# Optimization experiments

Measured on AMD Instinct MI355X. Metric: run time of the kernel, lower is better.

The kernel has to match this reference:

```python
import jax, jax.numpy as jnp
import numpy as np

H = 256          # hidden_dim
NH = 4           # num_heads
HD = H // NH     # head_dim = 64
EPS = 1e-5


def _ln(x, g, b):
    m = jnp.mean(x, axis=-1, keepdims=True)
    v = jnp.mean(jnp.square(x - m), axis=-1, keepdims=True)
    return (x - m) * jax.lax.rsqrt(v + EPS) * g + b


def _mha1(q_in, kv_in, in_proj_w, in_proj_b, out_w, out_b):
    # Single-query / single-key multihead attention (seq_len == 1 on both sides).
    # q_in, kv_in: [B, H]
    Wq, Wk, Wv = jnp.split(in_proj_w, 3, axis=0)   # each [H, H]
    bq, bk, bv = jnp.split(in_proj_b, 3, axis=0)
    B = q_in.shape[0]
    q = (q_in @ Wq.T + bq).reshape(B, NH, HD)
    k = (kv_in @ Wk.T + bk).reshape(B, NH, HD)
    v = (kv_in @ Wv.T + bv).reshape(B, NH, HD)
    scores = jnp.sum(q * k, axis=-1, keepdims=True) / jnp.sqrt(jnp.float32(HD))  # [B,NH,1]
    w = jax.nn.softmax(scores, axis=-1)  # softmax over 1 key -> all ones
    out = (w * v).reshape(B, H)
    return out @ out_w.T + out_b


def setup_inputs() -> dict:
    key = jax.random.key(0)
    ks = jax.random.split(key, 16)
    B, BIO, TXT, NC = 65536, 32, 768, 2
    s = lambda n: 1.0 / np.sqrt(n)
    return {
        "bio": jax.random.normal(ks[0], (B, BIO), jnp.float32),
        "text": jax.random.normal(ks[1], (B, TXT), jnp.float32),
        "bio_w": jax.random.normal(ks[2], (H, BIO), jnp.float32) * s(BIO),
        "bio_b": jnp.zeros((H,), jnp.float32),
        "text_w": jax.random.normal(ks[3], (H, TXT), jnp.float32) * s(TXT),
        "text_b": jnp.zeros((H,), jnp.float32),
        "ln_bio_g": jnp.ones((H,), jnp.float32),
        "ln_bio_b": jnp.zeros((H,), jnp.float32),
        "ln_text_g": jnp.ones((H,), jnp.float32),
        "ln_text_b": jnp.zeros((H,), jnp.float32),
        "in_proj_w": jax.random.normal(ks[4], (3 * H, H), jnp.float32) * s(H),
        "in_proj_b": jnp.zeros((3 * H,), jnp.float32),
        "out_w": jax.random.normal(ks[5], (H, H), jnp.float32) * s(H),
        "out_b": jnp.zeros((H,), jnp.float32),
        "cls1_w": jax.random.normal(ks[6], (H, 2 * H), jnp.float32) * s(2 * H),
        "cls1_b": jnp.zeros((H,), jnp.float32),
        "cls_ln_g": jnp.ones((H,), jnp.float32),
        "cls_ln_b": jnp.zeros((H,), jnp.float32),
        "cls2_w": jax.random.normal(ks[7], (NC, H), jnp.float32) * s(H),
        "cls2_b": jnp.zeros((NC,), jnp.float32),
    }


def reference(bio, text, bio_w, bio_b, text_w, text_b, ln_bio_g, ln_bio_b,
              ln_text_g, ln_text_b, in_proj_w, in_proj_b, out_w, out_b,
              cls1_w, cls1_b, cls_ln_g, cls_ln_b, cls2_w, cls2_b):
    b = _ln(bio @ bio_w.T + bio_b, ln_bio_g, ln_bio_b)      # [B, H]
    t = _ln(text @ text_w.T + text_b, ln_text_g, ln_text_b)  # [B, H]
    attn_bio = _mha1(b, t, in_proj_w, in_proj_b, out_w, out_b)
    attn_text = _mha1(t, b, in_proj_w, in_proj_b, out_w, out_b)
    fused = jnp.concatenate([attn_bio, attn_text], axis=-1)  # [B, 2H]
    h = jax.nn.relu(_ln(fused @ cls1_w.T + cls1_b, cls_ln_g, cls_ln_b))
    return h @ cls2_w.T + cls2_b
```

## Files before the change

### kernel.cpp

```cpp
#include <hip/hip_runtime.h>

typedef __attribute__((ext_vector_type(4))) float f4;
typedef __attribute__((ext_vector_type(8))) short s8;

#define EPS 1e-5f

__device__ __forceinline__ unsigned short f2bf(float f) {
    union { float f; unsigned u; } v; v.f = f;
    unsigned u = v.u;
    return (unsigned short)((u + 0x7fffu + ((u >> 16) & 1u)) >> 16);
}
__device__ __forceinline__ unsigned pack2(float a, float b) {
    return (unsigned)f2bf(a) | ((unsigned)f2bf(b) << 16);
}

__global__ __launch_bounds__(256) void k_prep_fl(const float* __restrict__ text_w,
                                                 const float* __restrict__ bio_w,
                                                 unsigned short* __restrict__ twFL,
                                                 unsigned short* __restrict__ bwFL) {
    int b = blockIdx.x, t = threadIdx.x;
    if (b < 96) {
        int idx = b * 256 + t;
        int ksg = idx >> 10;
        int rem = idx & 1023;
        int ct = rem >> 6, lane = rem & 63;
        int n  = ct * 16 + (lane & 15);
        int k0 = ksg * 32 + ((lane >> 4) << 3);
        const float* src = &text_w[n * 768 + k0];
        f4 a = *(const f4*)src, c = *(const f4*)(src + 4);
        unsigned* dst = (unsigned*)&twFL[idx * 8];
        dst[0] = pack2(a[0], a[1]); dst[1] = pack2(a[2], a[3]);
        dst[2] = pack2(c[0], c[1]); dst[3] = pack2(c[2], c[3]);
    } else {
        int idx = (b - 96) * 256 + t;
        int ct = idx >> 6, lane = idx & 63;
        int n  = ct * 16 + (lane & 15);
        int k0 = (lane >> 4) << 3;
        const float* src = &bio_w[n * 32 + k0];
        f4 a = *(const f4*)src, c = *(const f4*)(src + 4);
        unsigned* dst = (unsigned*)&bwFL[idx * 8];
        dst[0] = pack2(a[0], a[1]); dst[1] = pack2(a[2], a[3]);
        dst[2] = pack2(c[0], c[1]); dst[3] = pack2(c[2], c[3]);
    }
}

__global__ __launch_bounds__(256) void k_prep_A(const float* __restrict__ out_w,
                                                const float* __restrict__ in_proj_w,
                                                const float* __restrict__ in_proj_b,
                                                const float* __restrict__ out_b,
                                                float* __restrict__ A,
                                                float* __restrict__ cvec) {
    __shared__ float srow[256];
    __shared__ float red[256];
    int i = blockIdx.x, j = threadIdx.x;
    srow[j] = out_w[i * 256 + j];
    __syncthreads();
    float acc = 0.f;
#pragma unroll 8
    for (int k = 0; k < 256; k++)
        acc = fmaf(srow[k], in_proj_w[(512 + k) * 256 + j], acc);
    A[i * 256 + j] = acc;
    red[j] = srow[j] * in_proj_b[512 + j];
    __syncthreads();
    for (int s = 128; s > 0; s >>= 1) {
        if (j < s) red[j] += red[j + s];
        __syncthreads();
    }
    if (j == 0) cvec[i] = red[0] + out_b[i];
}

__global__ __launch_bounds__(256) void k_prep_PQ(const float* __restrict__ cls1_w,
                                                 const float* __restrict__ cls1_b,
                                                 const float* __restrict__ A,
                                                 const float* __restrict__ cvec,
                                                 const float* __restrict__ ln_text_g,
                                                 const float* __restrict__ ln_text_b,
                                                 const float* __restrict__ ln_bio_g,
                                                 const float* __restrict__ ln_bio_b,
                                                 unsigned short* __restrict__ pqFL,
                                                 float* __restrict__ dvec) {
    __shared__ float w1[256], w2[256], red[256];
    int i = blockIdx.x, j = threadIdx.x;
    w1[j] = cls1_w[i * 512 + j];
    w2[j] = cls1_w[i * 512 + 256 + j];
    __syncthreads();
    float rp = 0.f, rq = 0.f;
#pragma unroll 4
    for (int k = 0; k < 256; k++) {
        float a = A[k * 256 + j];
        rp = fmaf(w1[k], a, rp);
        rq = fmaf(w2[k], a, rq);
    }
    int ct   = i >> 4;
    int lane = (i & 15) | (((j >> 3) & 3) << 4);
    int jj   = j & 7;
    int ks1  = j >> 5;
    pqFL[(((ks1     ) * 16 + ct) * 64 + lane) * 8 + jj] = f2bf(rp * ln_text_g[j]);
    pqFL[(((ks1 + 8 ) * 16 + ct) * 64 + lane) * 8 + jj] = f2bf(rq * ln_bio_g[j]);
    red[j] = rp * ln_text_b[j] + rq * ln_bio_b[j] + (w1[j] + w2[j]) * cvec[j];
    __syncthreads();
    for (int s = 128; s > 0; s >>= 1) {
        if (j < s) red[j] += red[j + s];
        __syncthreads();
    }
    if (j == 0) dvec[i] = red[0] + cls1_b[i];
}

__global__ __launch_bounds__(256, 3) void k_main(
    const float* __restrict__ bio, const float* __restrict__ text,
    const float* __restrict__ bio_b, const float* __restrict__ text_b,
    const float* __restrict__ cls_ln_g, const float* __restrict__ cls_ln_b,
    const float* __restrict__ cls2_w, const float* __restrict__ cls2_b,
    const unsigned short* __restrict__ twFL, const unsigned short* __restrict__ bwFL,
    const unsigned short* __restrict__ pqFL, const float* __restrict__ dvec,
    float* __restrict__ out)
{
    __shared__ __align__(16) unsigned short s_n[32][520];
    __shared__ __align__(16) unsigned short s_x[32][200];
    __shared__ __align__(16) unsigned short s_b[32][40];
    __shared__ float s_red[4][32][2];

    const int tid  = threadIdx.x;
    const int w    = tid >> 6;
    const int lane = tid & 63;
    const int q    = lane >> 4;
    const int lr   = lane & 15;
    const int R0   = blockIdx.x * 32;

    f4 acc[2][4];
    float s1[2][4], s2[2][4];
    float m_[2][4], iv_[2][4];

    {
        int row = tid >> 3, c4 = tid & 7;
        f4 v = *(const f4*)&bio[(size_t)(R0 + row) * 32 + c4 * 4];
        uint2 p; p.x = pack2(v[0], v[1]); p.y = pack2(v[2], v[3]);
        *(uint2*)&s_b[row][c4 * 4] = p;
    }
    __syncthreads();

#pragma unroll
    for (int rt = 0; rt < 2; rt++)
#pragma unroll
        for (int c = 0; c < 4; c++) acc[rt][c] = (f4){0.f, 0.f, 0.f, 0.f};
    {
        s8 bfr[4];
#pragma unroll
        for (int c = 0; c < 4; c++)
            bfr[c] = *(const s8*)&bwFL[((w * 4 + c) * 64 + lane) * 8];
#pragma unroll
        for (int rt = 0; rt < 2; rt++) {
            s8 afr = *(const s8*)&s_b[rt * 16 + lr][q * 8];
#pragma unroll
            for (int c = 0; c < 4; c++)
                acc[rt][c] = __builtin_amdgcn_mfma_f32_16x16x32_bf16(afr, bfr[c], acc[rt][c], 0, 0, 0);
        }
    }
#pragma unroll
    for (int rt = 0; rt < 2; rt++)
#pragma unroll
        for (int r = 0; r < 4; r++) { s1[rt][r] = 0.f; s2[rt][r] = 0.f; }
#pragma unroll
    for (int rt = 0; rt < 2; rt++)
#pragma unroll
        for (int c = 0; c < 4; c++) {
            float bb = bio_b[w * 64 + c * 16 + lr];
#pragma unroll
            for (int r = 0; r < 4; r++) {
                float x = acc[rt][c][r] + bb;
                acc[rt][c][r] = x;
                s1[rt][r] += x; s2[rt][r] += x * x;
            }
        }
#pragma unroll
    for (int off = 1; off < 16; off <<= 1)
#pragma unroll
        for (int rt = 0; rt < 2; rt++)
#pragma unroll
            for (int r = 0; r < 4; r++) {
                s1[rt][r] += __shfl_xor(s1[rt][r], off, 64);
                s2[rt][r] += __shfl_xor(s2[rt][r], off, 64);
            }
    if (lr == 0)
#pragma unroll
        for (int rt = 0; rt < 2; rt++)
#pragma unroll
            for (int r = 0; r < 4; r++) {
                int row = rt * 16 + q * 4 + r;
                s_red[w][row][0] = s1[rt][r];
                s_red[w][row][1] = s2[rt][r];
            }
    __syncthreads();
#pragma unroll
    for (int rt = 0; rt < 2; rt++)
#pragma unroll
        for (int r = 0; r < 4; r++) {
            int row = rt * 16 + q * 4 + r;
            float t1 = s_red[0][row][0] + s_red[1][row][0] + s_red[2][row][0] + s_red[3][row][0];
            float t2 = s_red[0][row][1] + s_red[1][row][1] + s_red[2][row][1] + s_red[3][row][1];
            float mm = t1 * (1.f / 256.f);
            float vv = t2 * (1.f / 256.f) - mm * mm;
            m_[rt][r]  = mm;
            iv_[rt][r] = rsqrtf(vv + EPS);
        }
#pragma unroll
    for (int rt = 0; rt < 2; rt++)
#pragma unroll
        for (int c = 0; c < 4; c++) {
            int col = w * 64 + c * 16 + lr;
#pragma unroll
            for (int r = 0; r < 4; r++)
                s_n[rt * 16 + q * 4 + r][256 + col] = f2bf((acc[rt][c][r] - m_[rt][r]) * iv_[rt][r]);
        }

#pragma unroll
    for (int rt = 0; rt < 2; rt++)
#pragma unroll
        for (int c = 0; c < 4; c++) acc[rt][c] = (f4){0.f, 0.f, 0.f, 0.f};

    for (int kc = 0; kc < 768; kc += 192) {
        __syncthreads();
#pragma unroll
        for (int i = 0; i < 6; i++) {
            int idx = tid + i * 256;
            int row = idx / 48;
            int c4  = idx % 48;
            f4 v = *(const f4*)&text[(size_t)(R0 + row) * 768 + kc + c4 * 4];
            uint2 p; p.x = pack2(v[0], v[1]); p.y = pack2(v[2], v[3]);
            *(uint2*)&s_x[row][c4 * 4] = p;
        }
        __syncthreads();
        int ksg0 = kc >> 5;
#pragma unroll
        for (int ks = 0; ks < 6; ks++) {
            s8 bfr[4];
#pragma unroll
            for (int c = 0; c < 4; c++)
                bfr[c] = *(const s8*)&twFL[(((ksg0 + ks) * 16 + w * 4 + c) * 64 + lane) * 8];
#pragma unroll
            for (int rt = 0; rt < 2; rt++) {
                s8 afr = *(const s8*)&s_x[rt * 16 + lr][ks * 32 + q * 8];
#pragma unroll
                for (int c = 0; c < 4; c++)
                    acc[rt][c] = __builtin_amdgcn_mfma_f32_16x16x32_bf16(afr, bfr[c], acc[rt][c], 0, 0, 0);
            }
        }
    }
#pragma unroll
    for (int rt = 0; rt < 2; rt++)
#pragma unroll
        for (int r = 0; r < 4; r++) { s1[rt][r] = 0.f; s2[rt][r] = 0.f; }
#pragma unroll
    for (int rt = 0; rt < 2; rt++)
#pragma unroll
        for (int c = 0; c < 4; c++) {
            float bb = text_b[w * 64 + c * 16 + lr];
#pragma unroll
            for (int r = 0; r < 4; r++) {
                float x = acc[rt][c][r] + bb;
                acc[rt][c][r] = x;
                s1[rt][r] += x; s2[rt][r] += x * x;
            }
        }
#pragma unroll
    for (int off = 1; off < 16; off <<= 1)
#pragma unroll
        for (int rt = 0; rt < 2; rt++)
#pragma unroll
            for (int r = 0; r < 4; r++) {
                s1[rt][r] += __shfl_xor(s1[rt][r], off, 64);
                s2[rt][r] += __shfl_xor(s2[rt][r], off, 64);
            }
    __syncthreads();
    if (lr == 0)
#pragma unroll
        for (int rt = 0; rt < 2; rt++)
#pragma unroll
            for (int r = 0; r < 4; r++) {
                int row = rt * 16 + q * 4 + r;
                s_red[w][row][0] = s1[rt][r];
                s_red[w][row][1] = s2[rt][r];
            }
    __syncthreads();
#pragma unroll
    for (int rt = 0; rt < 2; rt++)
#pragma unroll
        for (int r = 0; r < 4; r++) {
            int row = rt * 16 + q * 4 + r;
            float t1 = s_red[0][row][0] + s_red[1][row][0] + s_red[2][row][0] + s_red[3][row][0];
            float t2 = s_red[0][row][1] + s_red[1][row][1] + s_red[2][row][1] + s_red[3][row][1];
            float mm = t1 * (1.f / 256.f);
            float vv = t2 * (1.f / 256.f) - mm * mm;
            m_[rt][r]  = mm;
            iv_[rt][r] = rsqrtf(vv + EPS);
        }
#pragma unroll
    for (int rt = 0; rt < 2; rt++)
#pragma unroll
        for (int c = 0; c < 4; c++) {
            int col = w * 64 + c * 16 + lr;
#pragma unroll
            for (int r = 0; r < 4; r++)
                s_n[rt * 16 + q * 4 + r][col] = f2bf((acc[rt][c][r] - m_[rt][r]) * iv_[rt][r]);
        }
    __syncthreads();

#pragma unroll
    for (int rt = 0; rt < 2; rt++)
#pragma unroll
        for (int c = 0; c < 4; c++) {
            float dv = dvec[w * 64 + c * 16 + lr];
            acc[rt][c] = (f4){dv, dv, dv, dv};
        }
#pragma unroll 4
    for (int ks = 0; ks < 16; ks++) {
        s8 bfr[4];
#pragma unroll
        for (int c = 0; c < 4; c++)
            bfr[c] = *(const s8*)&pqFL[((ks * 16 + w * 4 + c) * 64 + lane) * 8];
#pragma unroll
        for (int rt = 0; rt < 2; rt++) {
            s8 afr = *(const s8*)&s_n[rt * 16 + lr][ks * 32 + q * 8];
#pragma unroll
            for (int c = 0; c < 4; c++)
                acc[rt][c] = __builtin_amdgcn_mfma_f32_16x16x32_bf16(afr, bfr[c], acc[rt][c], 0, 0, 0);
        }
    }

#pragma unroll
    for (int rt = 0; rt < 2; rt++)
#pragma unroll
        for (int r = 0; r < 4; r++) { s1[rt][r] = 0.f; s2[rt][r] = 0.f; }
#pragma unroll
    for (int rt = 0; rt < 2; rt++)
#pragma unroll
        for (int c = 0; c < 4; c++)
#pragma unroll
            for (int r = 0; r < 4; r++) {
                float x = acc[rt][c][r];
                s1[rt][r] += x; s2[rt][r] += x * x;
            }
#pragma unroll
    for (int off = 1; off < 16; off <<= 1)
#pragma unroll
        for (int rt = 0; rt < 2; rt++)
#pragma unroll
            for (int r = 0; r < 4; r++) {
                s1[rt][r] += __shfl_xor(s1[rt][r], off, 64);
                s2[rt][r] += __shfl_xor(s2[rt][r], off, 64);
            }
    if (lr == 0)
#pragma unroll
        for (int rt = 0; rt < 2; rt++)
#pragma unroll
            for (int r = 0; r < 4; r++) {
                int row = rt * 16 + q * 4 + r;
                s_red[w][row][0] = s1[rt][r];
                s_red[w][row][1] = s2[rt][r];
            }
    __syncthreads();
#pragma unroll
    for (int rt = 0; rt < 2; rt++)
#pragma unroll
        for (int r = 0; r < 4; r++) {
            int row = rt * 16 + q * 4 + r;
            float t1 = s_red[0][row][0] + s_red[1][row][0] + s_red[2][row][0] + s_red[3][row][0];
            float t2 = s_red[0][row][1] + s_red[1][row][1] + s_red[2][row][1] + s_red[3][row][1];
            float mm = t1 * (1.f / 256.f);
            float vv = t2 * (1.f / 256.f) - mm * mm;
            m_[rt][r]  = mm;
            iv_[rt][r] = rsqrtf(vv + EPS);
        }
    float po0[2][4], po1[2][4];
#pragma unroll
    for (int rt = 0; rt < 2; rt++)
#pragma unroll
        for (int r = 0; r < 4; r++) { po0[rt][r] = 0.f; po1[rt][r] = 0.f; }
#pragma unroll
    for (int rt = 0; rt < 2; rt++)
#pragma unroll
        for (int c = 0; c < 4; c++) {
            int col = w * 64 + c * 16 + lr;
            float gg = cls_ln_g[col], bb = cls_ln_b[col];
            float c0 = cls2_w[col],   c1 = cls2_w[256 + col];
#pragma unroll
            for (int r = 0; r < 4; r++) {
                float h = fmaxf((acc[rt][c][r] - m_[rt][r]) * iv_[rt][r] * gg + bb, 0.f);
                po0[rt][r] = fmaf(h, c0, po0[rt][r]);
                po1[rt][r] = fmaf(h, c1, po1[rt][r]);
            }
        }
#pragma unroll
    for (int off = 1; off < 16; off <<= 1)
#pragma unroll
        for (int rt = 0; rt < 2; rt++)
#pragma unroll
            for (int r = 0; r < 4; r++) {
                po0[rt][r] += __shfl_xor(po0[rt][r], off, 64);
                po1[rt][r] += __shfl_xor(po1[rt][r], off, 64);
            }
    __syncthreads();
    if (lr == 0)
#pragma unroll
        for (int rt = 0; rt < 2; rt++)
#pragma unroll
            for (int r = 0; r < 4; r++) {
                int row = rt * 16 + q * 4 + r;
                s_red[w][row][0] = po0[rt][r];
                s_red[w][row][1] = po1[rt][r];
            }
    __syncthreads();
    if (tid < 64) {
        int row = tid >> 1, comp = tid & 1;
        float v = s_red[0][row][comp] + s_red[1][row][comp] +
                  s_red[2][row][comp] + s_red[3][row][comp];
        out[(size_t)(R0 + row) * 2 + comp] = v + cls2_b[comp];
    }
}

extern "C" void kernel_launch(void* const* d_in, const int* in_sizes, int n_in,
                              void* d_out, int out_size, void* d_ws, size_t ws_size,
                              hipStream_t stream) {
    const float* bio       = (const float*)d_in[0];
    const float* text      = (const float*)d_in[1];
    const float* bio_w     = (const float*)d_in[2];
    const float* bio_b     = (const float*)d_in[3];
    const float* text_w    = (const float*)d_in[4];
    const float* text_b    = (const float*)d_in[5];
    const float* ln_bio_g  = (const float*)d_in[6];
    const float* ln_bio_b  = (const float*)d_in[7];
    const float* ln_text_g = (const float*)d_in[8];
    const float* ln_text_b = (const float*)d_in[9];
    const float* in_proj_w = (const float*)d_in[10];
    const float* in_proj_b = (const float*)d_in[11];
    const float* out_w     = (const float*)d_in[12];
    const float* out_b     = (const float*)d_in[13];
    const float* cls1_w    = (const float*)d_in[14];
    const float* cls1_b    = (const float*)d_in[15];
    const float* cls_ln_g  = (const float*)d_in[16];
    const float* cls_ln_b  = (const float*)d_in[17];
    const float* cls2_w    = (const float*)d_in[18];
    const float* cls2_b    = (const float*)d_in[19];
    float* out = (float*)d_out;

    float* ws   = (float*)d_ws;
    float* A    = ws;
    float* cvec = ws + 65536;
    float* dvec = ws + 65792;
    unsigned short* us   = (unsigned short*)(ws + 66048);
    unsigned short* twFL = us;
    unsigned short* bwFL = us + 196608;
    unsigned short* pqFL = us + 204800;

    k_prep_fl<<<100, 256, 0, stream>>>(text_w, bio_w, twFL, bwFL);
    k_prep_A <<<256, 256, 0, stream>>>(out_w, in_proj_w, in_proj_b, out_b, A, cvec);
    k_prep_PQ<<<256, 256, 0, stream>>>(cls1_w, cls1_b, A, cvec,
                                       ln_text_g, ln_text_b, ln_bio_g, ln_bio_b,
                                       pqFL, dvec);

    int nrows = in_sizes[0] / 32;
    k_main<<<nrows / 32, 256, 0, stream>>>(bio, text, bio_b, text_b,
                                           cls_ln_g, cls_ln_b, cls2_w, cls2_b,
                                           twFL, bwFL, pqFL, dvec, out);
}
```

Before: 407.3 us.

## Double rows per block, prefetch text chunks into registers, merge prep kernels

The main kernel now handles 64 rows per 512-thread block, with two row-halves of four column-slice waves each. The next 192-column text chunk is prefetched into registers while the current chunk is multiplied, and text staging reuses the s_n buffer, dropping the separate s_x and s_b buffers. Bio inputs are loaded straight into MFMA fragments instead of going through LDS. The first two prep kernels are merged into one launch and some unroll factors are raised. The aim is to hide global load latency and cut launch overhead, at the cost of higher register pressure and a larger LDS footprint per block.

Measured after the change: 397.3 us. 2.5% less time.

```diff
diff --git a/kernel.cpp b/kernel.cpp
--- a/kernel.cpp
+++ b/kernel.cpp
@@ -13,11 +13,23 @@
 __device__ __forceinline__ unsigned pack2(float a, float b) {
     return (unsigned)f2bf(a) | ((unsigned)f2bf(b) << 16);
 }
-
-__global__ __launch_bounds__(256) void k_prep_fl(const float* __restrict__ text_w,
-                                                 const float* __restrict__ bio_w,
-                                                 unsigned short* __restrict__ twFL,
-                                                 unsigned short* __restrict__ bwFL) {
+__device__ __forceinline__ s8 pack8(f4 a, f4 b) {
+    union { s8 v; unsigned u[4]; } r;
+    r.u[0] = pack2(a[0], a[1]); r.u[1] = pack2(a[2], a[3]);
+    r.u[2] = pack2(b[0], b[1]); r.u[3] = pack2(b[2], b[3]);
+    return r.v;
+}
+
+__global__ __launch_bounds__(256) void k_prep1(const float* __restrict__ text_w,
+                                               const float* __restrict__ bio_w,
+                                               const float* __restrict__ out_w,
+                                               const float* __restrict__ in_proj_w,
+                                               const float* __restrict__ in_proj_b,
+                                               const float* __restrict__ out_b,
+                                               unsigned short* __restrict__ twFL,
+                                               unsigned short* __restrict__ bwFL,
+                                               float* __restrict__ A,
+                                               float* __restrict__ cvec) {
     int b = blockIdx.x, t = threadIdx.x;
     if (b < 96) {
         int idx = b * 256 + t;
@@ -31,7 +43,7 @@
         unsigned* dst = (unsigned*)&twFL[idx * 8];
         dst[0] = pack2(a[0], a[1]); dst[1] = pack2(a[2], a[3]);
         dst[2] = pack2(c[0], c[1]); dst[3] = pack2(c[2], c[3]);
-    } else {
+    } else if (b < 100) {
         int idx = (b - 96) * 256 + t;
         int ct = idx >> 6, lane = idx & 63;
         int n  = ct * 16 + (lane & 15);
@@ -41,32 +53,25 @@
         unsigned* dst = (unsigned*)&bwFL[idx * 8];
         dst[0] = pack2(a[0], a[1]); dst[1] = pack2(a[2], a[3]);
         dst[2] = pack2(c[0], c[1]); dst[3] = pack2(c[2], c[3]);
-    }
-}
-
-__global__ __launch_bounds__(256) void k_prep_A(const float* __restrict__ out_w,
-                                                const float* __restrict__ in_proj_w,
-                                                const float* __restrict__ in_proj_b,
-                                                const float* __restrict__ out_b,
-                                                float* __restrict__ A,
-                                                float* __restrict__ cvec) {
-    __shared__ float srow[256];
-    __shared__ float red[256];
-    int i = blockIdx.x, j = threadIdx.x;
-    srow[j] = out_w[i * 256 + j];
-    __syncthreads();
-    float acc = 0.f;
-#pragma unroll 8
-    for (int k = 0; k < 256; k++)
-        acc = fmaf(srow[k], in_proj_w[(512 + k) * 256 + j], acc);
-    A[i * 256 + j] = acc;
-    red[j] = srow[j] * in_proj_b[512 + j];
-    __syncthreads();
-    for (int s = 128; s > 0; s >>= 1) {
-        if (j < s) red[j] += red[j + s];
+    } else {
+        __shared__ float srow[256];
+        __shared__ float red[256];
+        int i = b - 100, j = t;
+        srow[j] = out_w[i * 256 + j];
         __syncthreads();
-    }
-    if (j == 0) cvec[i] = red[0] + out_b[i];
+        float acc = 0.f;
+#pragma unroll 16
+        for (int k = 0; k < 256; k++)
+            acc = fmaf(srow[k], in_proj_w[(512 + k) * 256 + j], acc);
+        A[i * 256 + j] = acc;
+        red[j] = srow[j] * in_proj_b[512 + j];
+        __syncthreads();
+        for (int s = 128; s > 0; s >>= 1) {
+            if (j < s) red[j] += red[j + s];
+            __syncthreads();
+        }
+        if (j == 0) cvec[i] = red[0] + out_b[i];
+    }
 }
 
 __global__ __launch_bounds__(256) void k_prep_PQ(const float* __restrict__ cls1_w,
@@ -85,7 +90,7 @@
     w2[j] = cls1_w[i * 512 + 256 + j];
     __syncthreads();
     float rp = 0.f, rq = 0.f;
-#pragma unroll 4
+#pragma unroll 8
     for (int k = 0; k < 256; k++) {
         float a = A[k * 256 + j];
         rp = fmaf(w1[k], a, rp);
@@ -106,7 +111,7 @@
     if (j == 0) dvec[i] = red[0] + cls1_b[i];
 }
 
-__global__ __launch_bounds__(256, 3) void k_main(
+__global__ __launch_bounds__(512, 4) void k_main(
     const float* __restrict__ bio, const float* __restrict__ text,
     const float* __restrict__ bio_b, const float* __restrict__ text_b,
     const float* __restrict__ cls_ln_g, const float* __restrict__ cls_ln_b,
@@ -115,46 +120,55 @@
     const unsigned short* __restrict__ pqFL, const float* __restrict__ dvec,
     float* __restrict__ out)
 {
-    __shared__ __align__(16) unsigned short s_n[32][520];
-    __shared__ __align__(16) unsigned short s_x[32][200];
-    __shared__ __align__(16) unsigned short s_b[32][40];
-    __shared__ float s_red[4][32][2];
+    __shared__ __align__(16) unsigned short s_n[64][520];
+    __shared__ float s_red[4][64][2];
 
     const int tid  = threadIdx.x;
-    const int w    = tid >> 6;
+    const int wv   = tid >> 6;
+    const int cs   = wv & 3;
+    const int rh   = wv >> 2;
     const int lane = tid & 63;
     const int q    = lane >> 4;
     const int lr   = lane & 15;
-    const int R0   = blockIdx.x * 32;
+    const int R0   = blockIdx.x * 64;
 
     f4 acc[2][4];
-    float s1[2][4], s2[2][4];
-    float m_[2][4], iv_[2][4];
-
-    {
-        int row = tid >> 3, c4 = tid & 7;
-        f4 v = *(const f4*)&bio[(size_t)(R0 + row) * 32 + c4 * 4];
-        uint2 p; p.x = pack2(v[0], v[1]); p.y = pack2(v[2], v[3]);
-        *(uint2*)&s_b[row][c4 * 4] = p;
-    }
-    __syncthreads();
+    float s1[2][4], s2[2][4], m_[2][4], iv_[2][4];
+
+    f4 bioA[2], bioB[2];
+#pragma unroll
+    for (int rt = 0; rt < 2; rt++) {
+        const float* p = &bio[(size_t)(R0 + rh * 32 + rt * 16 + lr) * 32 + q * 8];
+        bioA[rt] = *(const f4*)p;
+        bioB[rt] = *(const f4*)(p + 4);
+    }
+    s8 bfrb[4];
+#pragma unroll
+    for (int c = 0; c < 4; c++)
+        bfrb[c] = *(const s8*)&bwFL[((cs * 4 + c) * 64 + lane) * 8];
+
+    int toff[6], soff[6];
+    f4 tpre[6];
+#pragma unroll
+    for (int i = 0; i < 6; i++) {
+        int idx = tid + i * 512;
+        int row = idx / 48;
+        int c4  = idx - row * 48;
+        toff[i] = (R0 + row) * 768 + c4 * 4;
+        soff[i] = row * 520 + c4 * 4;
+        tpre[i] = *(const f4*)&text[(size_t)toff[i]];
+    }
 
 #pragma unroll
     for (int rt = 0; rt < 2; rt++)
 #pragma unroll
         for (int c = 0; c < 4; c++) acc[rt][c] = (f4){0.f, 0.f, 0.f, 0.f};
-    {
-        s8 bfr[4];
+#pragma unroll
+    for (int rt = 0; rt < 2; rt++) {
+        s8 af = pack8(bioA[rt], bioB[rt]);
 #pragma unroll
         for (int c = 0; c < 4; c++)
-            bfr[c] = *(const s8*)&bwFL[((w * 4 + c) * 64 + lane) * 8];
-#pragma unroll
-        for (int rt = 0; rt < 2; rt++) {
-            s8 afr = *(const s8*)&s_b[rt * 16 + lr][q * 8];
-#pragma unroll
-            for (int c = 0; c < 4; c++)
-                acc[rt][c] = __builtin_amdgcn_mfma_f32_16x16x32_bf16(afr, bfr[c], acc[rt][c], 0, 0, 0);
-        }
+            acc[rt][c] = __builtin_amdgcn_mfma_f32_16x16x32_bf16(af, bfrb[c], acc[rt][c], 0, 0, 0);
     }
 #pragma unroll
     for (int rt = 0; rt < 2; rt++)
@@ -164,7 +178,7 @@
     for (int rt = 0; rt < 2; rt++)
 #pragma unroll
         for (int c = 0; c < 4; c++) {
-            float bb = bio_b[w * 64 + c * 16 + lr];
+            float bb = bio_b[cs * 64 + c * 16 + lr];
 #pragma unroll
             for (int r = 0; r < 4; r++) {
                 float x = acc[rt][c][r] + bb;
@@ -186,16 +200,16 @@
         for (int rt = 0; rt < 2; rt++)
 #pragma unroll
             for (int r = 0; r < 4; r++) {
-                int row = rt * 16 + q * 4 + r;
-                s_red[w][row][0] = s1[rt][r];
-                s_red[w][row][1] = s2[rt][r];
+                int row = rh * 32 + rt * 16 + q * 4 + r;
+                s_red[cs][row][0] = s1[rt][r];
+                s_red[cs][row][1] = s2[rt][r];
             }
     __syncthreads();
 #pragma unroll
     for (int rt = 0; rt < 2; rt++)
 #pragma unroll
         for (int r = 0; r < 4; r++) {
-            int row = rt * 16 + q * 4 + r;
+            int row = rh * 32 + rt * 16 + q * 4 + r;
             float t1 = s_red[0][row][0] + s_red[1][row][0] + s_red[2][row][0] + s_red[3][row][0];
             float t2 = s_red[0][row][1] + s_red[1][row][1] + s_red[2][row][1] + s_red[3][row][1];
             float mm = t1 * (1.f / 256.f);
@@ -207,10 +221,11 @@
     for (int rt = 0; rt < 2; rt++)
 #pragma unroll
         for (int c = 0; c < 4; c++) {
-            int col = w * 64 + c * 16 + lr;
+            int col = cs * 64 + c * 16 + lr;
 #pragma unroll
             for (int r = 0; r < 4; r++)
-                s_n[rt * 16 + q * 4 + r][256 + col] = f2bf((acc[rt][c][r] - m_[rt][r]) * iv_[rt][r]);
+                s_n[rh * 32 + rt * 16 + q * 4 + r][256 + col] =
+                    f2bf((acc[rt][c][r] - m_[rt][r]) * iv_[rt][r]);
         }
 
 #pragma unroll
@@ -218,31 +233,31 @@
 #pragma unroll
         for (int c = 0; c < 4; c++) acc[rt][c] = (f4){0.f, 0.f, 0.f, 0.f};
 
-    for (int kc = 0; kc < 768; kc += 192) {
+    for (int ch = 0; ch < 4; ch++) {
+        if (ch) __syncthreads();
+#pragma unroll
+        for (int i = 0; i < 6; i++) {
+            uint2 p; p.x = pack2(tpre[i][0], tpre[i][1]); p.y = pack2(tpre[i][2], tpre[i][3]);
+            *(uint2*)&((unsigned short*)s_n)[soff[i]] = p;
+        }
+        if (ch < 3)
+#pragma unroll
+            for (int i = 0; i < 6; i++)
+                tpre[i] = *(const f4*)&text[(size_t)(toff[i] + (ch + 1) * 192)];
         __syncthreads();
-#pragma unroll
-        for (int i = 0; i < 6; i++) {
-            int idx = tid + i * 256;
-            int row = idx / 48;
-            int c4  = idx % 48;
-            f4 v = *(const f4*)&text[(size_t)(R0 + row) * 768 + kc + c4 * 4];
-            uint2 p; p.x = pack2(v[0], v[1]); p.y = pack2(v[2], v[3]);
-            *(uint2*)&s_x[row][c4 * 4] = p;
-        }
-        __syncthreads();
-        int ksg0 = kc >> 5;
+        int ksg0 = ch * 6;
 #pragma unroll
         for (int ks = 0; ks < 6; ks++) {
             s8 bfr[4];
 #pragma unroll
             for (int c = 0; c < 4; c++)
-                bfr[c] = *(const s8*)&twFL[(((ksg0 + ks) * 16 + w * 4 + c) * 64 + lane) * 8];
+                bfr[c] = *(const s8*)&twFL[(((ksg0 + ks) * 16 + cs * 4 + c) * 64 + lane) * 8];
 #pragma unroll
             for (int rt = 0; rt < 2; rt++) {
-                s8 afr = *(const s8*)&s_x[rt * 16 + lr][ks * 32 + q * 8];
+                s8 af = *(const s8*)&s_n[rh * 32 + rt * 16 + lr][ks * 32 + q * 8];
 #pragma unroll
                 for (int c = 0; c < 4; c++)
-                    acc[rt][c] = __builtin_amdgcn_mfma_f32_16x16x32_bf16(afr, bfr[c], acc[rt][c], 0, 0, 0);
+                    acc[rt][c] = __builtin_amdgcn_mfma_f32_16x16x32_bf16(af, bfr[c], acc[rt][c], 0, 0, 0);
             }
         }
     }
@@ -254,7 +269,7 @@
     for (int rt = 0; rt < 2; rt++)
 #pragma unroll
         for (int c = 0; c < 4; c++) {
-            float bb = text_b[w * 64 + c * 16 + lr];
+            float bb = text_b[cs * 64 + c * 16 + lr];
 #pragma unroll
             for (int r = 0; r < 4; r++) {
                 float x = acc[rt][c][r] + bb;
@@ -277,16 +292,16 @@
         for (int rt = 0; rt < 2; rt++)
 #pragma unroll
             for (int r = 0; r < 4; r++) {
-                int row = rt * 16 + q * 4 + r;
-                s_red[w][row][0] = s1[rt][r];
-                s_red[w][row][1] = s2[rt][r];
+                int row = rh * 32 + rt * 16 + q * 4 + r;
+                s_red[cs][row][0] = s1[rt][r];
+                s_red[cs][row][1] = s2[rt][r];
             }
     __syncthreads();
 #pragma unroll
     for (int rt = 0; rt < 2; rt++)
 #pragma unroll
         for (int r = 0; r < 4; r++) {
-            int row = rt * 16 + q * 4 + r;
+            int row = rh * 32 + rt * 16 + q * 4 + r;
             float t1 = s_red[0][row][0] + s_red[1][row][0] + s_red[2][row][0] + s_red[3][row][0];
             float t2 = s_red[0][row][1] + s_red[1][row][1] + s_red[2][row][1] + s_red[3][row][1];
             float mm = t1 * (1.f / 256.f);
@@ -298,18 +313,19 @@
     for (int rt = 0; rt < 2; rt++)
 #pragma unroll
         for (int c = 0; c < 4; c++) {
-            int col = w * 64 + c * 16 + lr;
+            int col = cs * 64 + c * 16 + lr;
 #pragma unroll
             for (int r = 0; r < 4; r++)
-                s_n[rt * 16 + q * 4 + r][col] = f2bf((acc[rt][c][r] - m_[rt][r]) * iv_[rt][r]);
-        }
-    __syncthreads();
-
-#pragma unroll
-    for (int rt = 0; rt < 2; rt++)
-#pragma unroll
-        for (int c = 0; c < 4; c++) {
-            float dv = dvec[w * 64 + c * 16 + lr];
+                s_n[rh * 32 + rt * 16 + q * 4 + r][col] =
+                    f2bf((acc[rt][c][r] - m_[rt][r]) * iv_[rt][r]);
+        }
+    __syncthreads();
+
+#pragma unroll
+    for (int rt = 0; rt < 2; rt++)
+#pragma unroll
+        for (int c = 0; c < 4; c++) {
+            float dv = dvec[cs * 64 + c * 16 + lr];
             acc[rt][c] = (f4){dv, dv, dv, dv};
         }
 #pragma unroll 4
@@ -317,13 +333,13 @@
         s8 bfr[4];
 #pragma unroll
         for (int c = 0; c < 4; c++)
-            bfr[c] = *(const s8*)&pqFL[((ks * 16 + w * 4 + c) * 64 + lane) * 8];
+            bfr[c] = *(const s8*)&pqFL[((ks * 16 + cs * 4 + c) * 64 + lane) * 8];
 #pragma unroll
         for (int rt = 0; rt < 2; rt++) {
-            s8 afr = *(const s8*)&s_n[rt * 16 + lr][ks * 32 + q * 8];
+            s8 af = *(const s8*)&s_n[rh * 32 + rt * 16 + lr][ks * 32 + q * 8];
 #pragma unroll
             for (int c = 0; c < 4; c++)
-                acc[rt][c] = __builtin_amdgcn_mfma_f32_16x16x32_bf16(afr, bfr[c], acc[rt][c], 0, 0, 0);
+                acc[rt][c] = __builtin_amdgcn_mfma_f32_16x16x32_bf16(af, bfr[c], acc[rt][c], 0, 0, 0);
         }
     }
 
@@ -349,21 +365,22 @@
                 s1[rt][r] += __shfl_xor(s1[rt][r], off, 64);
                 s2[rt][r] += __shfl_xor(s2[rt][r], off, 64);
             }
+    __syncthreads();
     if (lr == 0)
 #pragma unroll
         for (int rt = 0; rt < 2; rt++)
 #pragma unroll
             for (int r = 0; r < 4; r++) {
-                int row = rt * 16 + q * 4 + r;
-                s_red[w][row][0] = s1[rt][r];
-                s_red[w][row][1] = s2[rt][r];
+                int row = rh * 32 + rt * 16 + q * 4 + r;
+                s_red[cs][row][0] = s1[rt][r];
+                s_red[cs][row][1] = s2[rt][r];
             }
     __syncthreads();
 #pragma unroll
     for (int rt = 0; rt < 2; rt++)
 #pragma unroll
         for (int r = 0; r < 4; r++) {
-            int row = rt * 16 + q * 4 + r;
+            int row = rh * 32 + rt * 16 + q * 4 + r;
             float t1 = s_red[0][row][0] + s_red[1][row][0] + s_red[2][row][0] + s_red[3][row][0];
             float t2 = s_red[0][row][1] + s_red[1][row][1] + s_red[2][row][1] + s_red[3][row][1];
             float mm = t1 * (1.f / 256.f);
@@ -380,7 +397,7 @@
     for (int rt = 0; rt < 2; rt++)
 #pragma unroll
         for (int c = 0; c < 4; c++) {
-            int col = w * 64 + c * 16 + lr;
+            int col = cs * 64 + c * 16 + lr;
             float gg = cls_ln_g[col], bb = cls_ln_b[col];
             float c0 = cls2_w[col],   c1 = cls2_w[256 + col];
 #pragma unroll
@@ -405,12 +422,12 @@
         for (int rt = 0; rt < 2; rt++)
 #pragma unroll
             for (int r = 0; r < 4; r++) {
-                int row = rt * 16 + q * 4 + r;
-                s_red[w][row][0] = po0[rt][r];
-                s_red[w][row][1] = po1[rt][r];
-            }
-    __syncthreads();
-    if (tid < 64) {
+                int row = rh * 32 + rt * 16 + q * 4 + r;
+                s_red[cs][row][0] = po0[rt][r];
+                s_red[cs][row][1] = po1[rt][r];
+            }
+    __syncthreads();
+    if (tid < 128) {
         int row = tid >> 1, comp = tid & 1;
         float v = s_red[0][row][comp] + s_red[1][row][comp] +
                   s_red[2][row][comp] + s_red[3][row][comp];
@@ -452,14 +469,14 @@
     unsigned short* bwFL = us + 196608;
     unsigned short* pqFL = us + 204800;
 
-    k_prep_fl<<<100, 256, 0, stream>>>(text_w, bio_w, twFL, bwFL);
-    k_prep_A <<<256, 256, 0, stream>>>(out_w, in_proj_w, in_proj_b, out_b, A, cvec);
+    k_prep1  <<<356, 256, 0, stream>>>(text_w, bio_w, out_w, in_proj_w, in_proj_b, out_b,
+                                       twFL, bwFL, A, cvec);
     k_prep_PQ<<<256, 256, 0, stream>>>(cls1_w, cls1_b, A, cvec,
                                        ln_text_g, ln_text_b, ln_bio_g, ln_bio_b,
                                        pqFL, dvec);
 
     int nrows = in_sizes[0] / 32;
-    k_main<<<nrows / 32, 256, 0, stream>>>(bio, text, bio_b, text_b,
+    k_main<<<nrows / 64, 512, 0, stream>>>(bio, text, bio_b, text_b,
                                            cls_ln_g, cls_ln_b, cls2_w, cls2_b,
                                            twFL, bwFL, pqFL, dvec, out);
 }
```
